# Optimization experiments

Measured on AMD Instinct MI355X. Metric: run time of the kernel, lower is better.

The kernel has to match this reference:

```python
import jax, jax.numpy as jnp
import numpy as np

N = 50000   # nodes
E = 800000  # edges (avg degree 16)
F_IN = 128
D_HID = 128
N_CLASS = 40


def setup_inputs() -> dict:
    key = jax.random.key(0)
    ks = jax.random.split(key, 10)
    s = 0.05
    return {
        "x": jax.random.normal(ks[0], (N, F_IN), jnp.float32),
        "edge_index": jax.random.randint(ks[1], (2, E), 0, N, dtype=jnp.int32),
        "W_in": jax.random.normal(ks[2], (F_IN, D_HID), jnp.float32) * s,
        "b_in": jnp.zeros((D_HID,), jnp.float32),
        "W1": jax.random.normal(ks[3], (D_HID, D_HID), jnp.float32) * s,
        "b1": jnp.zeros((D_HID,), jnp.float32),
        "W2": jax.random.normal(ks[4], (D_HID, D_HID), jnp.float32) * s,
        "b2": jnp.zeros((D_HID,), jnp.float32),
        "W_out": jax.random.normal(ks[5], (D_HID, N_CLASS), jnp.float32) * s,
        "b_out": jnp.zeros((N_CLASS,), jnp.float32),
    }


def _gcn_norm(edge_index, num_nodes):
    # Add self loops, compute symmetric normalization D^-1/2 (A+I) D^-1/2.
    loop = jnp.arange(num_nodes, dtype=edge_index.dtype)
    src = jnp.concatenate([edge_index[0], loop])
    dst = jnp.concatenate([edge_index[1], loop])
    deg = jnp.zeros((num_nodes,), jnp.float32).at[dst].add(1.0)
    dinv = jnp.where(deg > 0, jax.lax.rsqrt(deg), 0.0)
    norm = dinv[src] * dinv[dst]  # [E+N]
    return src, dst, norm


def _gcn_conv(h, W, b, src, dst, norm, num_nodes):
    # transform then sparse aggregate (gather-scale-scatter)
    h = h @ W                                   # [N, d]
    msg = h[src] * norm[:, None]                # [E+N, d]
    agg = jax.ops.segment_sum(msg, dst, num_segments=num_nodes)
    return agg + b


def reference(x, edge_index, W_in, b_in, W1, b1, W2, b2, W_out, b_out):
    num_nodes = x.shape[0]
    src, dst, norm = _gcn_norm(edge_index, num_nodes)
    h = _gcn_conv(x, W_in, b_in, src, dst, norm, num_nodes)
    # eval mode: dropout is identity
    h = jax.nn.relu(_gcn_conv(h, W1, b1, src, dst, norm, num_nodes))
    h = jax.nn.relu(_gcn_conv(h, W2, b2, src, dst, norm, num_nodes))
    out = h @ W_out + b_out
    return jax.nn.log_softmax(out, axis=1)
```

## Files before the change

kernel.cpp:

```cpp
#include <hip/hip_runtime.h>
#include <hip/hip_bf16.h>
#include <math.h>

typedef unsigned int uint;
typedef unsigned short ushort;
typedef __attribute__((ext_vector_type(8))) short short8;
typedef __attribute__((ext_vector_type(4))) float f32x4;

__device__ __forceinline__ float bf_lo(uint u) { return __uint_as_float(u << 16); }
__device__ __forceinline__ float bf_hi(uint u) { return __uint_as_float(u & 0xffff0000u); }
__device__ __forceinline__ ushort f2bf(float f) {
  __hip_bfloat16 h = __float2bfloat16(f);
  return *reinterpret_cast<ushort*>(&h);
}
__device__ __forceinline__ uint pack2(float a, float b) {
  return (uint)f2bf(a) | ((uint)f2bf(b) << 16);
}

__global__ __launch_bounds__(256) void k_pcnt(
    const float* __restrict__ W_in, const float* __restrict__ W1,
    const float* __restrict__ W2, ushort* __restrict__ Wt,
    const int* __restrict__ edges, int* __restrict__ cnt8, int E, int n)
{
  int b = blockIdx.x;
  if (b < 24) {
    const float* W = (b < 8) ? W_in : (b < 16) ? W1 : W2;
    ushort* dst = Wt + (size_t)(b >> 3) * 16384;
    int id = (b & 7) * 256 + threadIdx.x;
    int col = id >> 4, kc = id & 15;
    const float* src = W + (size_t)(kc * 8) * 128 + col;
    uint4 pk;
    pk.x = pack2(src[0],       src[128]);
    pk.y = pack2(src[2 * 128], src[3 * 128]);
    pk.z = pack2(src[4 * 128], src[5 * 128]);
    pk.w = pack2(src[6 * 128], src[7 * 128]);
    ((uint4*)dst)[id] = pk;
  } else {
    int cb = b - 24;
    int* my = cnt8 + (size_t)(cb & 7) * n;
    int stride = ((int)gridDim.x - 24) * 256;
    for (int e = cb * 256 + threadIdx.x; e < E; e += stride)
      atomicAdd(&my[edges[E + e]], 1);
  }
}

__global__ void k_scan1(const int* __restrict__ cnt8, int* __restrict__ cnt,
                        int* __restrict__ incl, int* __restrict__ bsum,
                        float* __restrict__ dinv, int n) {
  __shared__ int s[256];
  int tid = threadIdx.x;
  int gid = blockIdx.x * 256 + tid;
  int x = 0;
  if (gid < n) {
    #pragma unroll
    for (int p = 0; p < 8; ++p) x += cnt8[(size_t)p * n + gid];
    cnt[gid] = x;
    dinv[gid] = rsqrtf((float)x + 1.0f);
  }
  s[tid] = x;
  __syncthreads();
  #pragma unroll
  for (int off = 1; off < 256; off <<= 1) {
    int t = (tid >= off) ? s[tid - off] : 0;
    __syncthreads();
    x += t; s[tid] = x;
    __syncthreads();
  }
  incl[gid] = x;
  if (tid == 255) bsum[blockIdx.x] = x;
}

__global__ void k_scan3(const int* __restrict__ incl, const int* __restrict__ cnt,
                        const int* __restrict__ bsum, int* __restrict__ offs,
                        int* __restrict__ curs, int n, int E, int nb) {
  __shared__ int sb[256];
  int tid = threadIdx.x;
  sb[tid] = (tid < (int)blockIdx.x && tid < nb) ? bsum[tid] : 0;
  __syncthreads();
  #pragma unroll
  for (int off = 128; off; off >>= 1) {
    if (tid < off) sb[tid] += sb[tid + off];
    __syncthreads();
  }
  int base = sb[0];
  int gid = blockIdx.x * 256 + tid;
  if (gid < n) {
    int v = incl[gid] - cnt[gid] + base;
    offs[gid] = v;
    curs[gid] = v;
  }
  if (gid == 0) offs[n] = E;
}

__global__ __launch_bounds__(256) void k_gf(
    const float* __restrict__ A, const ushort* __restrict__ Wt,
    const float* __restrict__ dinv, ushort* __restrict__ T, int n, int gb,
    const int* __restrict__ edges, int* __restrict__ curs,
    int* __restrict__ csr, int E, int npp, int nbp)
{
  __shared__ ushort sW[128 * 128];
  int tid = threadIdx.x;

  if ((int)blockIdx.x >= gb) {
    int b2 = blockIdx.x - gb;
    int part = b2 & 7;
    int lo = part * npp, hi = lo + npp;
    for (int e = (b2 >> 3) * 256 + tid; e < E; e += nbp * 256) {
      int d = edges[E + e];
      if (d >= lo && d < hi) {
        int s = edges[e];
        int pos = atomicAdd(&curs[d], 1);
        csr[pos] = s;
      }
    }
    return;
  }

  {
    const uint4* Wt4 = (const uint4*)Wt;
    uint4* sW4 = (uint4*)sW;
    #pragma unroll
    for (int j = 0; j < 8; ++j) {
      int id = j * 256 + tid;
      int col = id >> 4, kc = id & 15;
      sW4[(col << 4) | (kc ^ (col & 7))] = Wt4[id];
    }
  }
  __syncthreads();

  int wid = tid >> 6, lane = tid & 63;
  int lr = lane & 15, lg = lane >> 4;
  int rbase = blockIdx.x * 64 + wid * 16;
  int arow = rbase + lr;
  bool valid = arow < n;

  f32x4 acc[8];
  #pragma unroll
  for (int cf = 0; cf < 8; ++cf) acc[cf] = (f32x4){0.f, 0.f, 0.f, 0.f};

  #pragma unroll
  for (int ks = 0; ks < 4; ++ks) {
    short8 a = {};
    if (valid) {
      const float4* Af = (const float4*)(A + (size_t)arow * 128) + (ks * 4 + lg) * 2;
      float4 u = Af[0], w = Af[1];
      union { uint4 u4; short8 s8; } cv;
      cv.u4.x = pack2(u.x, u.y); cv.u4.y = pack2(u.z, u.w);
      cv.u4.z = pack2(w.x, w.y); cv.u4.w = pack2(w.z, w.w);
      a = cv.s8;
    }
    int kc = (ks << 2) | lg;
    #pragma unroll
    for (int cf = 0; cf < 8; ++cf) {
      int col = (cf << 4) | lr;
      const short8* bp = (const short8*)sW + ((col << 4) | (kc ^ (lr & 7)));
      acc[cf] = __builtin_amdgcn_mfma_f32_16x16x32_bf16(a, *bp, acc[cf], 0, 0, 0);
    }
  }

  #pragma unroll
  for (int v = 0; v < 4; ++v) {
    int row = rbase + (lg << 2) + v;
    if (row < n) {
      float s = dinv[row];
      ushort* dst = T + (size_t)row * 128 + lr;
      #pragma unroll
      for (int cf = 0; cf < 8; ++cf) dst[cf << 4] = f2bf(acc[cf][v] * s);
    }
  }
}

__global__ __launch_bounds__(256) void k_gemm(
    const ushort* __restrict__ Ap, const ushort* __restrict__ Wt,
    const float* __restrict__ dinv, ushort* __restrict__ T, int n)
{
  __shared__ ushort sW[128 * 128];
  int tid = threadIdx.x;
  {
    const uint4* Wt4 = (const uint4*)Wt;
    uint4* sW4 = (uint4*)sW;
    #pragma unroll
    for (int j = 0; j < 8; ++j) {
      int id = j * 256 + tid;
      int col = id >> 4, kc = id & 15;
      sW4[(col << 4) | (kc ^ (col & 7))] = Wt4[id];
    }
  }
  __syncthreads();

  int wid = tid >> 6, lane = tid & 63;
  int lr = lane & 15, lg = lane >> 4;
  int rbase = blockIdx.x * 64 + wid * 16;
  int arow = rbase + lr;
  bool valid = arow < n;

  f32x4 acc[8];
  #pragma unroll
  for (int cf = 0; cf < 8; ++cf) acc[cf] = (f32x4){0.f, 0.f, 0.f, 0.f};

  #pragma unroll
  for (int ks = 0; ks < 4; ++ks) {
    short8 a = {};
    if (valid) a = ((const short8*)(Ap + (size_t)arow * 128))[ks * 4 + lg];
    int kc = (ks << 2) | lg;
    #pragma unroll
    for (int cf = 0; cf < 8; ++cf) {
      int col = (cf << 4) | lr;
      const short8* bp = (const short8*)sW + ((col << 4) | (kc ^ (lr & 7)));
      acc[cf] = __builtin_amdgcn_mfma_f32_16x16x32_bf16(a, *bp, acc[cf], 0, 0, 0);
    }
  }

  #pragma unroll
  for (int v = 0; v < 4; ++v) {
    int row = rbase + (lg << 2) + v;
    if (row < n) {
      float s = dinv[row];
      ushort* dst = T + (size_t)row * 128 + lr;
      #pragma unroll
      for (int cf = 0; cf < 8; ++cf) dst[cf << 4] = f2bf(acc[cf][v] * s);
    }
  }
}

__global__ __launch_bounds__(256) void k_agg(
    const ushort* __restrict__ T, const int* __restrict__ offs,
    const int* __restrict__ csr, const float* __restrict__ dinv,
    const float* __restrict__ bias, ushort* __restrict__ H, int n, int relu)
{
  int u = (blockIdx.x << 2) + (threadIdx.x >> 6);
  if (u >= n) return;
  int lane = threadIdx.x & 63;
  const uint* Tu = (const uint*)T;
  uint su = Tu[(size_t)u * 64 + lane];
  float ax = bf_lo(su), ay = bf_hi(su);
  int e0 = offs[u], e1 = offs[u + 1];
  int deg = e1 - e0;
  int dcap = deg > 64 ? 64 : deg;
  int eid = (lane < deg) ? csr[e0 + lane] : 0;
  int j = 0;
  for (; j + 8 <= dcap; j += 8) {
    int s0 = __shfl(eid, j);     int s1 = __shfl(eid, j + 1);
    int s2 = __shfl(eid, j + 2); int s3 = __shfl(eid, j + 3);
    int s4 = __shfl(eid, j + 4); int s5 = __shfl(eid, j + 5);
    int s6 = __shfl(eid, j + 6); int s7 = __shfl(eid, j + 7);
    uint v0 = Tu[(size_t)s0 * 64 + lane];
    uint v1 = Tu[(size_t)s1 * 64 + lane];
    uint v2 = Tu[(size_t)s2 * 64 + lane];
    uint v3 = Tu[(size_t)s3 * 64 + lane];
    uint v4 = Tu[(size_t)s4 * 64 + lane];
    uint v5 = Tu[(size_t)s5 * 64 + lane];
    uint v6 = Tu[(size_t)s6 * 64 + lane];
    uint v7 = Tu[(size_t)s7 * 64 + lane];
    ax += ((bf_lo(v0) + bf_lo(v1)) + (bf_lo(v2) + bf_lo(v3))) +
          ((bf_lo(v4) + bf_lo(v5)) + (bf_lo(v6) + bf_lo(v7)));
    ay += ((bf_hi(v0) + bf_hi(v1)) + (bf_hi(v2) + bf_hi(v3))) +
          ((bf_hi(v4) + bf_hi(v5)) + (bf_hi(v6) + bf_hi(v7)));
  }
  for (; j < dcap; ++j) {
    int s = __shfl(eid, j);
    uint v = Tu[(size_t)s * 64 + lane];
    ax += bf_lo(v); ay += bf_hi(v);
  }
  for (int e = e0 + 64; e < e1; ++e) {
    uint v = Tu[(size_t)csr[e] * 64 + lane];
    ax += bf_lo(v); ay += bf_hi(v);
  }
  float du = dinv[u];
  float2 b2 = *(const float2*)(bias + (lane << 1));
  float ox = fmaf(ax, du, b2.x);
  float oy = fmaf(ay, du, b2.y);
  if (relu) { ox = fmaxf(ox, 0.f); oy = fmaxf(oy, 0.f); }
  ((uint*)H)[(size_t)u * 64 + lane] = pack2(ox, oy);
}

__global__ __launch_bounds__(256) void k_head(
    const ushort* __restrict__ H, const float* __restrict__ Wo,
    const float* __restrict__ bo, float* __restrict__ out, int n)
{
  __shared__ float sWo[128 * 40];
  __shared__ float sX[128 * 64];
  int tid = threadIdx.x;
  int rbase = blockIdx.x * 64;

  {
    const float4* Wo4 = (const float4*)Wo;
    float4* sWo4 = (float4*)sWo;
    #pragma unroll
    for (int i = 0; i < 5; ++i) sWo4[i * 256 + tid] = Wo4[i * 256 + tid];
  }
  {
    const uint4* H4 = (const uint4*)H;
    #pragma unroll
    for (int j = 0; j < 4; ++j) {
      int id = j * 256 + tid;
      int r = id & 63, kc8 = id >> 6;
      int row = rbase + r;
      uint4 v = make_uint4(0u, 0u, 0u, 0u);
      if (row < n) v = H4[(size_t)row * 16 + kc8];
      float f[8] = {bf_lo(v.x), bf_hi(v.x), bf_lo(v.y), bf_hi(v.y),
                    bf_lo(v.z), bf_hi(v.z), bf_lo(v.w), bf_hi(v.w)};
      #pragma unroll
      for (int j2 = 0; j2 < 8; ++j2) {
        int k = kc8 * 8 + j2;
        int swz = ((k >> 2) & 7) << 2;
        sX[k * 64 + (r ^ swz)] = f[j2];
      }
    }
  }
  __syncthreads();

  int cg = tid & 7;
  int rg = tid >> 3;
  float bj[5];
  #pragma unroll
  for (int j = 0; j < 5; ++j) bj[j] = bo[cg * 5 + j];
  float acc[2][5];
  #pragma unroll
  for (int i = 0; i < 2; ++i)
    #pragma unroll
    for (int j = 0; j < 5; ++j) acc[i][j] = bj[j];

  #pragma unroll 4
  for (int k = 0; k < 128; ++k) {
    int swz = ((k >> 2) & 7) << 2;
    float2 xv = *(const float2*)(sX + k * 64 + ((rg << 1) ^ swz));
    const float* wr = sWo + k * 40 + cg * 5;
    float w0 = wr[0], w1 = wr[1], w2 = wr[2], w3 = wr[3], w4 = wr[4];
    acc[0][0] = fmaf(xv.x, w0, acc[0][0]);
    acc[0][1] = fmaf(xv.x, w1, acc[0][1]);
    acc[0][2] = fmaf(xv.x, w2, acc[0][2]);
    acc[0][3] = fmaf(xv.x, w3, acc[0][3]);
    acc[0][4] = fmaf(xv.x, w4, acc[0][4]);
    acc[1][0] = fmaf(xv.y, w0, acc[1][0]);
    acc[1][1] = fmaf(xv.y, w1, acc[1][1]);
    acc[1][2] = fmaf(xv.y, w2, acc[1][2]);
    acc[1][3] = fmaf(xv.y, w3, acc[1][3]);
    acc[1][4] = fmaf(xv.y, w4, acc[1][4]);
  }

  #pragma unroll
  for (int i = 0; i < 2; ++i) {
    int row = rbase + (rg << 1) + i;
    float m = acc[i][0];
    m = fmaxf(m, acc[i][1]); m = fmaxf(m, acc[i][2]);
    m = fmaxf(m, acc[i][3]); m = fmaxf(m, acc[i][4]);
    m = fmaxf(m, __shfl_xor(m, 1));
    m = fmaxf(m, __shfl_xor(m, 2));
    m = fmaxf(m, __shfl_xor(m, 4));
    float s = 0.f;
    #pragma unroll
    for (int j = 0; j < 5; ++j) s += __expf(acc[i][j] - m);
    s += __shfl_xor(s, 1);
    s += __shfl_xor(s, 2);
    s += __shfl_xor(s, 4);
    float ls = m + __logf(s);
    if (row < n) {
      float* dst = out + (size_t)row * 40 + cg * 5;
      #pragma unroll
      for (int j = 0; j < 5; ++j) dst[j] = acc[i][j] - ls;
    }
  }
}

extern "C" void kernel_launch(void* const* d_in, const int* in_sizes, int n_in,
                              void* d_out, int out_size, void* d_ws, size_t ws_size,
                              hipStream_t stream) {
  const float* x    = (const float*)d_in[0];
  const int*   edges= (const int*)d_in[1];
  const float* W_in = (const float*)d_in[2];
  const float* b_in = (const float*)d_in[3];
  const float* W1   = (const float*)d_in[4];
  const float* b1   = (const float*)d_in[5];
  const float* W2   = (const float*)d_in[6];
  const float* b2   = (const float*)d_in[7];
  const float* Wo   = (const float*)d_in[8];
  const float* bo   = (const float*)d_in[9];
  float* out = (float*)d_out;

  int N = in_sizes[0] / 128;
  int E = in_sizes[1] / 2;
  int NB = (N + 255) / 256;

  char* p = (char*)d_ws;
  auto alloc = [&](size_t bytes) {
    char* r = p; p += (bytes + 255) & ~(size_t)255; return r;
  };
  ushort* t   = (ushort*)alloc((size_t)N * 128 * 2);
  ushort* h   = (ushort*)alloc((size_t)N * 128 * 2);
  ushort* wt  = (ushort*)alloc(3 * 16384 * 2);
  int*   cnt8 = (int*)  alloc((size_t)N * 8 * 4);
  int*   cnt  = (int*)  alloc((size_t)N * 4);
  float* dinv = (float*)alloc((size_t)N * 4);
  int*   incl = (int*)  alloc((size_t)NB * 256 * 4);
  int*   bsum = (int*)  alloc(256 * 4);
  int*   offs = (int*)  alloc((size_t)(N + 1) * 4);
  int*   curs = (int*)  alloc((size_t)N * 4);
  int*   csr  = (int*)  alloc((size_t)E * 4);
  (void)ws_size; (void)n_in; (void)out_size;

  int NPP = (N + 7) / 8;
  int NBP = 512;
  int GB = (N + 63) / 64;
  int AB = (N + 3) / 4;

  hipMemsetAsync(cnt8, 0, (size_t)N * 8 * 4, stream);
  k_pcnt <<<24 + 2048, 256, 0, stream>>>(W_in, W1, W2, wt, edges, cnt8, E, N);
  k_scan1<<<NB, 256, 0, stream>>>(cnt8, cnt, incl, bsum, dinv, N);
  k_scan3<<<NB, 256, 0, stream>>>(incl, cnt, bsum, offs, curs, N, E, NB);
  k_gf   <<<GB + NBP * 8, 256, 0, stream>>>(x, wt, dinv, t, N, GB,
                                            edges, curs, csr, E, NPP, NBP);
  k_agg  <<<AB, 256, 0, stream>>>(t, offs, csr, dinv, b_in, h, N, 0);
  k_gemm <<<GB, 256, 0, stream>>>(h, wt + 16384, dinv, t, N);
  k_agg  <<<AB, 256, 0, stream>>>(t, offs, csr, dinv, b1, h, N, 1);
  k_gemm <<<GB, 256, 0, stream>>>(h, wt + 2 * 16384, dinv, t, N);
  k_agg  <<<AB, 256, 0, stream>>>(t, offs, csr, dinv, b2, h, N, 1);

  k_head <<<GB, 256, 0, stream>>>(h, Wo, bo, out, N);
}
```

Measured before the change: 235.1 us.

## Fuse output head into last aggregation and partition-interleave block-to-row mapping

Removes the separate head kernel by computing the 128x40 output projection and log-softmax inside the final aggregation kernel, one wavefront per node, which avoids writing and re-reading the last hidden layer. GEMM and aggregation blocks now map to rows via blockIdx&7 partitions padded to 64-row multiples. This likely aims to match the XCD round-robin scheduling so each die's L2 holds a contiguous slice of nodes. The CSR fill loop is unrolled 4x to issue more independent loads. The fused head reloads 20KB of Wo per 4-node block and leaves lanes 40-63 idle, which may cost more than the kernel and traffic it removes.

```diff
diff --git a/kernel.cpp b/kernel.cpp
--- a/kernel.cpp
+++ b/kernel.cpp
@@ -2,6 +2,7 @@
 #include <hip/hip_bf16.h>
 #include <math.h>
 
+#define NEG_INF (-3.402823466e38f)
 typedef unsigned int uint;
 typedef unsigned short ushort;
 typedef __attribute__((ext_vector_type(8))) short short8;
@@ -96,7 +97,7 @@
     const float* __restrict__ A, const ushort* __restrict__ Wt,
     const float* __restrict__ dinv, ushort* __restrict__ T, int n, int gb,
     const int* __restrict__ edges, int* __restrict__ curs,
-    int* __restrict__ csr, int E, int npp, int nbp)
+    int* __restrict__ csr, int E, int npart, int nbp)
 {
   __shared__ ushort sW[128 * 128];
   int tid = threadIdx.x;
@@ -104,14 +105,22 @@
   if ((int)blockIdx.x >= gb) {
     int b2 = blockIdx.x - gb;
     int part = b2 & 7;
-    int lo = part * npp, hi = lo + npp;
-    for (int e = (b2 >> 3) * 256 + tid; e < E; e += nbp * 256) {
+    int lo = part * npart, hi = lo + npart;
+    int stride = nbp * 256;
+    int e = (b2 >> 3) * 256 + tid;
+    for (; e + 3 * stride < E; e += 4 * stride) {
+      int d0 = edges[E + e];
+      int d1 = edges[E + e + stride];
+      int d2 = edges[E + e + 2 * stride];
+      int d3 = edges[E + e + 3 * stride];
+      if (d0 >= lo && d0 < hi) { int s = edges[e];              csr[atomicAdd(&curs[d0], 1)] = s; }
+      if (d1 >= lo && d1 < hi) { int s = edges[e + stride];     csr[atomicAdd(&curs[d1], 1)] = s; }
+      if (d2 >= lo && d2 < hi) { int s = edges[e + 2 * stride]; csr[atomicAdd(&curs[d2], 1)] = s; }
+      if (d3 >= lo && d3 < hi) { int s = edges[e + 3 * stride]; csr[atomicAdd(&curs[d3], 1)] = s; }
+    }
+    for (; e < E; e += stride) {
       int d = edges[E + e];
-      if (d >= lo && d < hi) {
-        int s = edges[e];
-        int pos = atomicAdd(&curs[d], 1);
-        csr[pos] = s;
-      }
+      if (d >= lo && d < hi) { int s = edges[e]; csr[atomicAdd(&curs[d], 1)] = s; }
     }
     return;
   }
@@ -130,7 +139,8 @@
 
   int wid = tid >> 6, lane = tid & 63;
   int lr = lane & 15, lg = lane >> 4;
-  int rbase = blockIdx.x * 64 + wid * 16;
+  int part = blockIdx.x & 7, local = blockIdx.x >> 3;
+  int rbase = part * npart + local * 64 + wid * 16;
   int arow = rbase + lr;
   bool valid = arow < n;
 
@@ -172,7 +182,7 @@
 
 __global__ __launch_bounds__(256) void k_gemm(
     const ushort* __restrict__ Ap, const ushort* __restrict__ Wt,
-    const float* __restrict__ dinv, ushort* __restrict__ T, int n)
+    const float* __restrict__ dinv, ushort* __restrict__ T, int n, int npart)
 {
   __shared__ ushort sW[128 * 128];
   int tid = threadIdx.x;
@@ -190,7 +200,8 @@
 
   int wid = tid >> 6, lane = tid & 63;
   int lr = lane & 15, lg = lane >> 4;
-  int rbase = blockIdx.x * 64 + wid * 16;
+  int part = blockIdx.x & 7, local = blockIdx.x >> 3;
+  int rbase = part * npart + local * 64 + wid * 16;
   int arow = rbase + lr;
   bool valid = arow < n;
 
@@ -223,143 +234,93 @@
   }
 }
 
+template <int RELU, int HEAD>
 __global__ __launch_bounds__(256) void k_agg(
     const ushort* __restrict__ T, const int* __restrict__ offs,
     const int* __restrict__ csr, const float* __restrict__ dinv,
-    const float* __restrict__ bias, ushort* __restrict__ H, int n, int relu)
+    const float* __restrict__ bias, ushort* __restrict__ H,
+    const float* __restrict__ Wo, const float* __restrict__ bo,
+    float* __restrict__ outp, int n, int npart)
 {
-  int u = (blockIdx.x << 2) + (threadIdx.x >> 6);
-  if (u >= n) return;
-  int lane = threadIdx.x & 63;
-  const uint* Tu = (const uint*)T;
-  uint su = Tu[(size_t)u * 64 + lane];
-  float ax = bf_lo(su), ay = bf_hi(su);
-  int e0 = offs[u], e1 = offs[u + 1];
-  int deg = e1 - e0;
-  int dcap = deg > 64 ? 64 : deg;
-  int eid = (lane < deg) ? csr[e0 + lane] : 0;
-  int j = 0;
-  for (; j + 8 <= dcap; j += 8) {
-    int s0 = __shfl(eid, j);     int s1 = __shfl(eid, j + 1);
-    int s2 = __shfl(eid, j + 2); int s3 = __shfl(eid, j + 3);
-    int s4 = __shfl(eid, j + 4); int s5 = __shfl(eid, j + 5);
-    int s6 = __shfl(eid, j + 6); int s7 = __shfl(eid, j + 7);
-    uint v0 = Tu[(size_t)s0 * 64 + lane];
-    uint v1 = Tu[(size_t)s1 * 64 + lane];
-    uint v2 = Tu[(size_t)s2 * 64 + lane];
-    uint v3 = Tu[(size_t)s3 * 64 + lane];
-    uint v4 = Tu[(size_t)s4 * 64 + lane];
-    uint v5 = Tu[(size_t)s5 * 64 + lane];
-    uint v6 = Tu[(size_t)s6 * 64 + lane];
-    uint v7 = Tu[(size_t)s7 * 64 + lane];
-    ax += ((bf_lo(v0) + bf_lo(v1)) + (bf_lo(v2) + bf_lo(v3))) +
-          ((bf_lo(v4) + bf_lo(v5)) + (bf_lo(v6) + bf_lo(v7)));
-    ay += ((bf_hi(v0) + bf_hi(v1)) + (bf_hi(v2) + bf_hi(v3))) +
-          ((bf_hi(v4) + bf_hi(v5)) + (bf_hi(v6) + bf_hi(v7)));
-  }
-  for (; j < dcap; ++j) {
-    int s = __shfl(eid, j);
-    uint v = Tu[(size_t)s * 64 + lane];
-    ax += bf_lo(v); ay += bf_hi(v);
-  }
-  for (int e = e0 + 64; e < e1; ++e) {
-    uint v = Tu[(size_t)csr[e] * 64 + lane];
-    ax += bf_lo(v); ay += bf_hi(v);
-  }
-  float du = dinv[u];
-  float2 b2 = *(const float2*)(bias + (lane << 1));
-  float ox = fmaf(ax, du, b2.x);
-  float oy = fmaf(ay, du, b2.y);
-  if (relu) { ox = fmaxf(ox, 0.f); oy = fmaxf(oy, 0.f); }
-  ((uint*)H)[(size_t)u * 64 + lane] = pack2(ox, oy);
-}
-
-__global__ __launch_bounds__(256) void k_head(
-    const ushort* __restrict__ H, const float* __restrict__ Wo,
-    const float* __restrict__ bo, float* __restrict__ out, int n)
-{
-  __shared__ float sWo[128 * 40];
-  __shared__ float sX[128 * 64];
-  int tid = threadIdx.x;
-  int rbase = blockIdx.x * 64;
-
-  {
-    const float4* Wo4 = (const float4*)Wo;
-    float4* sWo4 = (float4*)sWo;
-    #pragma unroll
-    for (int i = 0; i < 5; ++i) sWo4[i * 256 + tid] = Wo4[i * 256 + tid];
-  }
-  {
-    const uint4* H4 = (const uint4*)H;
-    #pragma unroll
-    for (int j = 0; j < 4; ++j) {
-      int id = j * 256 + tid;
-      int r = id & 63, kc8 = id >> 6;
-      int row = rbase + r;
-      uint4 v = make_uint4(0u, 0u, 0u, 0u);
-      if (row < n) v = H4[(size_t)row * 16 + kc8];
-      float f[8] = {bf_lo(v.x), bf_hi(v.x), bf_lo(v.y), bf_hi(v.y),
-                    bf_lo(v.z), bf_hi(v.z), bf_lo(v.w), bf_hi(v.w)};
+  int tid = threadIdx.x;
+  int lane = tid & 63, wid = tid >> 6;
+  int part = blockIdx.x & 7, local = blockIdx.x >> 3;
+  int u = part * npart + (local << 2) + wid;
+  if (!HEAD && u >= n) return;
+
+  float ox = 0.f, oy = 0.f;
+  if (u < n) {
+    const uint* Tu = (const uint*)T;
+    uint su = Tu[(size_t)u * 64 + lane];
+    float ax = bf_lo(su), ay = bf_hi(su);
+    int e0 = offs[u], e1 = offs[u + 1];
+    int deg = e1 - e0;
+    int dcap = deg > 64 ? 64 : deg;
+    int eid = (lane < deg) ? csr[e0 + lane] : 0;
+    int j = 0;
+    for (; j + 8 <= dcap; j += 8) {
+      int s0 = __shfl(eid, j);     int s1 = __shfl(eid, j + 1);
+      int s2 = __shfl(eid, j + 2); int s3 = __shfl(eid, j + 3);
+      int s4 = __shfl(eid, j + 4); int s5 = __shfl(eid, j + 5);
+      int s6 = __shfl(eid, j + 6); int s7 = __shfl(eid, j + 7);
+      uint v0 = Tu[(size_t)s0 * 64 + lane];
+      uint v1 = Tu[(size_t)s1 * 64 + lane];
+      uint v2 = Tu[(size_t)s2 * 64 + lane];
+      uint v3 = Tu[(size_t)s3 * 64 + lane];
+      uint v4 = Tu[(size_t)s4 * 64 + lane];
+      uint v5 = Tu[(size_t)s5 * 64 + lane];
+      uint v6 = Tu[(size_t)s6 * 64 + lane];
+      uint v7 = Tu[(size_t)s7 * 64 + lane];
+      ax += ((bf_lo(v0) + bf_lo(v1)) + (bf_lo(v2) + bf_lo(v3))) +
+            ((bf_lo(v4) + bf_lo(v5)) + (bf_lo(v6) + bf_lo(v7)));
+      ay += ((bf_hi(v0) + bf_hi(v1)) + (bf_hi(v2) + bf_hi(v3))) +
+            ((bf_hi(v4) + bf_hi(v5)) + (bf_hi(v6) + bf_hi(v7)));
+    }
+    for (; j < dcap; ++j) {
+      int s = __shfl(eid, j);
+      uint v = Tu[(size_t)s * 64 + lane];
+      ax += bf_lo(v); ay += bf_hi(v);
+    }
+    for (int e = e0 + 64; e < e1; ++e) {
+      uint v = Tu[(size_t)csr[e] * 64 + lane];
+      ax += bf_lo(v); ay += bf_hi(v);
+    }
+    float du = dinv[u];
+    float2 b2 = *(const float2*)(bias + (lane << 1));
+    ox = fmaf(ax, du, b2.x);
+    oy = fmaf(ay, du, b2.y);
+    if (RELU) { ox = fmaxf(ox, 0.f); oy = fmaxf(oy, 0.f); }
+  }
+
+  if constexpr (HEAD) {
+    __shared__ float sWo[128 * 40];
+    __shared__ float sH[4][128];
+    for (int i = tid; i < 1280; i += 256) ((float4*)sWo)[i] = ((const float4*)Wo)[i];
+    if (u < n) { sH[wid][lane * 2] = ox; sH[wid][lane * 2 + 1] = oy; }
+    __syncthreads();
+    if (u < n) {
+      int c = (lane < 40) ? lane : 0;
+      float a0 = 0.f, a1 = 0.f, a2 = 0.f, a3 = 0.f;
+      const float* hr = sH[wid];
+      #pragma unroll 8
+      for (int k = 0; k < 128; k += 4) {
+        a0 = fmaf(hr[k],     sWo[k * 40 + c],       a0);
+        a1 = fmaf(hr[k + 1], sWo[(k + 1) * 40 + c], a1);
+        a2 = fmaf(hr[k + 2], sWo[(k + 2) * 40 + c], a2);
+        a3 = fmaf(hr[k + 3], sWo[(k + 3) * 40 + c], a3);
+      }
+      float logit = (a0 + a1) + (a2 + a3) + bo[c];
+      float m = (lane < 40) ? logit : NEG_INF;
       #pragma unroll
-      for (int j2 = 0; j2 < 8; ++j2) {
-        int k = kc8 * 8 + j2;
-        int swz = ((k >> 2) & 7) << 2;
-        sX[k * 64 + (r ^ swz)] = f[j2];
-      }
-    }
-  }
-  __syncthreads();
-
-  int cg = tid & 7;
-  int rg = tid >> 3;
-  float bj[5];
-  #pragma unroll
-  for (int j = 0; j < 5; ++j) bj[j] = bo[cg * 5 + j];
-  float acc[2][5];
-  #pragma unroll
-  for (int i = 0; i < 2; ++i)
-    #pragma unroll
-    for (int j = 0; j < 5; ++j) acc[i][j] = bj[j];
-
-  #pragma unroll 4
-  for (int k = 0; k < 128; ++k) {
-    int swz = ((k >> 2) & 7) << 2;
-    float2 xv = *(const float2*)(sX + k * 64 + ((rg << 1) ^ swz));
-    const float* wr = sWo + k * 40 + cg * 5;
-    float w0 = wr[0], w1 = wr[1], w2 = wr[2], w3 = wr[3], w4 = wr[4];
-    acc[0][0] = fmaf(xv.x, w0, acc[0][0]);
-    acc[0][1] = fmaf(xv.x, w1, acc[0][1]);
-    acc[0][2] = fmaf(xv.x, w2, acc[0][2]);
-    acc[0][3] = fmaf(xv.x, w3, acc[0][3]);
-    acc[0][4] = fmaf(xv.x, w4, acc[0][4]);
-    acc[1][0] = fmaf(xv.y, w0, acc[1][0]);
-    acc[1][1] = fmaf(xv.y, w1, acc[1][1]);
-    acc[1][2] = fmaf(xv.y, w2, acc[1][2]);
-    acc[1][3] = fmaf(xv.y, w3, acc[1][3]);
-    acc[1][4] = fmaf(xv.y, w4, acc[1][4]);
-  }
-
-  #pragma unroll
-  for (int i = 0; i < 2; ++i) {
-    int row = rbase + (rg << 1) + i;
-    float m = acc[i][0];
-    m = fmaxf(m, acc[i][1]); m = fmaxf(m, acc[i][2]);
-    m = fmaxf(m, acc[i][3]); m = fmaxf(m, acc[i][4]);
-    m = fmaxf(m, __shfl_xor(m, 1));
-    m = fmaxf(m, __shfl_xor(m, 2));
-    m = fmaxf(m, __shfl_xor(m, 4));
-    float s = 0.f;
-    #pragma unroll
-    for (int j = 0; j < 5; ++j) s += __expf(acc[i][j] - m);
-    s += __shfl_xor(s, 1);
-    s += __shfl_xor(s, 2);
-    s += __shfl_xor(s, 4);
-    float ls = m + __logf(s);
-    if (row < n) {
-      float* dst = out + (size_t)row * 40 + cg * 5;
+      for (int o = 32; o; o >>= 1) m = fmaxf(m, __shfl_xor(m, o));
+      float ex = (lane < 40) ? __expf(logit - m) : 0.f;
+      float s = ex;
       #pragma unroll
-      for (int j = 0; j < 5; ++j) dst[j] = acc[i][j] - ls;
-    }
+      for (int o = 32; o; o >>= 1) s += __shfl_xor(s, o);
+      if (lane < 40) outp[(size_t)u * 40 + lane] = logit - m - __logf(s);
+    }
+  } else {
+    if (u < n) ((uint*)H)[(size_t)u * 64 + lane] = pack2(ox, oy);
   }
 }
 
@@ -399,22 +360,25 @@
   int*   csr  = (int*)  alloc((size_t)E * 4);
   (void)ws_size; (void)n_in; (void)out_size;
 
-  int NPP = (N + 7) / 8;
+  int NPART = (((N + 7) / 8 + 63) / 64) * 64;
+  int GBP = NPART / 64;
+  int GB  = GBP * 8;
+  int APP = NPART / 4;
+  int AB  = APP * 8;
   int NBP = 512;
-  int GB = (N + 63) / 64;
-  int AB = (N + 3) / 4;
 
   hipMemsetAsync(cnt8, 0, (size_t)N * 8 * 4, stream);
   k_pcnt <<<24 + 2048, 256, 0, stream>>>(W_in, W1, W2, wt, edges, cnt8, E, N);
   k_scan1<<<NB, 256, 0, stream>>>(cnt8, cnt, incl, bsum, dinv, N);
   k_scan3<<<NB, 256, 0, stream>>>(incl, cnt, bsum, offs, curs, N, E, NB);
   k_gf   <<<GB + NBP * 8, 256, 0, stream>>>(x, wt, dinv, t, N, GB,
-                                            edges, curs, csr, E, NPP, NBP);
-  k_agg  <<<AB, 256, 0, stream>>>(t, offs, csr, dinv, b_in, h, N, 0);
-  k_gemm <<<GB, 256, 0, stream>>>(h, wt + 16384, dinv, t, N);
-  k_agg  <<<AB, 256, 0, stream>>>(t, offs, csr, dinv, b1, h, N, 1);
-  k_gemm <<<GB, 256, 0, stream>>>(h, wt + 2 * 16384, dinv, t, N);
-  k_agg  <<<AB, 256, 0, stream>>>(t, offs, csr, dinv, b2, h, N, 1);
-
-  k_head <<<GB, 256, 0, stream>>>(h, Wo, bo, out, N);
-}
+                                            edges, curs, csr, E, NPART, NBP);
+  k_agg<0, 0><<<AB, 256, 0, stream>>>(t, offs, csr, dinv, b_in, h,
+                                      nullptr, nullptr, nullptr, N, NPART);
+  k_gemm <<<GB, 256, 0, stream>>>(h, wt + 16384, dinv, t, N, NPART);
+  k_agg<1, 0><<<AB, 256, 0, stream>>>(t, offs, csr, dinv, b1, h,
+                                      nullptr, nullptr, nullptr, N, NPART);
+  k_gemm <<<GB, 256, 0, stream>>>(h, wt + 2 * 16384, dinv, t, N, NPART);
+  k_agg<1, 1><<<AB, 256, 0, stream>>>(t, offs, csr, dinv, b2, nullptr,
+                                      Wo, bo, out, N, NPART);
+}
```

Result: slower. 256.8 us (+9.2%).

## Reorder fused CSR-fill/GEMM blocks, drop LDS weight staging, template ReLU

Applied to the files above, without the earlier changes.

In the fused k_gf kernel, the CSR scatter blocks now take the low block indices so they are dispatched first, and the GEMM blocks follow. The GEMM path no longer stages the weight matrix into a swizzled LDS tile and reads B fragments straight from global memory, which frees 32KB of shared memory per block and removes a barrier. The scatter loop is unrolled by four so more edge loads are in flight at once. k_agg takes the ReLU flag as a template parameter, which trades extra instantiations for removing a runtime branch. The risks are uncoalesced global loads for the weights, and GEMM blocks possibly waiting behind the long scatter phase.

```diff
diff --git a/kernel.cpp b/kernel.cpp
--- a/kernel.cpp
+++ b/kernel.cpp
@@ -2,6 +2,7 @@
 #include <hip/hip_bf16.h>
 #include <math.h>
 
+#define NEG_INF (-3.402823466e38f)
 typedef unsigned int uint;
 typedef unsigned short ushort;
 typedef __attribute__((ext_vector_type(8))) short short8;
@@ -94,43 +95,38 @@
 
 __global__ __launch_bounds__(256) void k_gf(
     const float* __restrict__ A, const ushort* __restrict__ Wt,
-    const float* __restrict__ dinv, ushort* __restrict__ T, int n, int gb,
+    const float* __restrict__ dinv, ushort* __restrict__ T, int n, int fb,
     const int* __restrict__ edges, int* __restrict__ curs,
     int* __restrict__ csr, int E, int npp, int nbp)
 {
-  __shared__ ushort sW[128 * 128];
   int tid = threadIdx.x;
 
-  if ((int)blockIdx.x >= gb) {
-    int b2 = blockIdx.x - gb;
+  if ((int)blockIdx.x < fb) {
+    int b2 = blockIdx.x;
     int part = b2 & 7;
     int lo = part * npp, hi = lo + npp;
-    for (int e = (b2 >> 3) * 256 + tid; e < E; e += nbp * 256) {
+    int stride = nbp * 256;
+    int e = (b2 >> 3) * 256 + tid;
+    for (; e + 3 * stride < E; e += 4 * stride) {
+      int d0 = edges[E + e];
+      int d1 = edges[E + e + stride];
+      int d2 = edges[E + e + 2 * stride];
+      int d3 = edges[E + e + 3 * stride];
+      if (d0 >= lo && d0 < hi) { int s = edges[e];              csr[atomicAdd(&curs[d0], 1)] = s; }
+      if (d1 >= lo && d1 < hi) { int s = edges[e + stride];     csr[atomicAdd(&curs[d1], 1)] = s; }
+      if (d2 >= lo && d2 < hi) { int s = edges[e + 2 * stride]; csr[atomicAdd(&curs[d2], 1)] = s; }
+      if (d3 >= lo && d3 < hi) { int s = edges[e + 3 * stride]; csr[atomicAdd(&curs[d3], 1)] = s; }
+    }
+    for (; e < E; e += stride) {
       int d = edges[E + e];
-      if (d >= lo && d < hi) {
-        int s = edges[e];
-        int pos = atomicAdd(&curs[d], 1);
-        csr[pos] = s;
-      }
+      if (d >= lo && d < hi) { int s = edges[e]; csr[atomicAdd(&curs[d], 1)] = s; }
     }
     return;
   }
-
-  {
-    const uint4* Wt4 = (const uint4*)Wt;
-    uint4* sW4 = (uint4*)sW;
-    #pragma unroll
-    for (int j = 0; j < 8; ++j) {
-      int id = j * 256 + tid;
-      int col = id >> 4, kc = id & 15;
-      sW4[(col << 4) | (kc ^ (col & 7))] = Wt4[id];
-    }
-  }
-  __syncthreads();
 
   int wid = tid >> 6, lane = tid & 63;
   int lr = lane & 15, lg = lane >> 4;
-  int rbase = blockIdx.x * 64 + wid * 16;
+  int rbase = ((int)blockIdx.x - fb) * 64 + wid * 16;
   int arow = rbase + lr;
   bool valid = arow < n;
 
@@ -153,7 +149,7 @@
     #pragma unroll
     for (int cf = 0; cf < 8; ++cf) {
       int col = (cf << 4) | lr;
-      const short8* bp = (const short8*)sW + ((col << 4) | (kc ^ (lr & 7)));
+      const short8* bp = (const short8*)Wt + ((col << 4) | kc);
       acc[cf] = __builtin_amdgcn_mfma_f32_16x16x32_bf16(a, *bp, acc[cf], 0, 0, 0);
     }
   }
@@ -223,10 +219,11 @@
   }
 }
 
+template <int RELU>
 __global__ __launch_bounds__(256) void k_agg(
     const ushort* __restrict__ T, const int* __restrict__ offs,
     const int* __restrict__ csr, const float* __restrict__ dinv,
-    const float* __restrict__ bias, ushort* __restrict__ H, int n, int relu)
+    const float* __restrict__ bias, ushort* __restrict__ H, int n)
 {
   int u = (blockIdx.x << 2) + (threadIdx.x >> 6);
   if (u >= n) return;
@@ -270,7 +267,7 @@
   float2 b2 = *(const float2*)(bias + (lane << 1));
   float ox = fmaf(ax, du, b2.x);
   float oy = fmaf(ay, du, b2.y);
-  if (relu) { ox = fmaxf(ox, 0.f); oy = fmaxf(oy, 0.f); }
+  if (RELU) { ox = fmaxf(ox, 0.f); oy = fmaxf(oy, 0.f); }
   ((uint*)H)[(size_t)u * 64 + lane] = pack2(ox, oy);
 }
 
@@ -401,20 +398,20 @@
 
   int NPP = (N + 7) / 8;
   int NBP = 512;
-  int GB = (N + 63) / 64;
-  int AB = (N + 3) / 4;
+  int FB  = NBP * 8;
+  int GB  = (N + 63) / 64;
+  int AB  = (N + 3) / 4;
 
   hipMemsetAsync(cnt8, 0, (size_t)N * 8 * 4, stream);
   k_pcnt <<<24 + 2048, 256, 0, stream>>>(W_in, W1, W2, wt, edges, cnt8, E, N);
   k_scan1<<<NB, 256, 0, stream>>>(cnt8, cnt, incl, bsum, dinv, N);
   k_scan3<<<NB, 256, 0, stream>>>(incl, cnt, bsum, offs, curs, N, E, NB);
-  k_gf   <<<GB + NBP * 8, 256, 0, stream>>>(x, wt, dinv, t, N, GB,
-                                            edges, curs, csr, E, NPP, NBP);
-  k_agg  <<<AB, 256, 0, stream>>>(t, offs, csr, dinv, b_in, h, N, 0);
+  k_gf   <<<FB + GB, 256, 0, stream>>>(x, wt, dinv, t, N, FB,
+                                       edges, curs, csr, E, NPP, NBP);
+  k_agg<0><<<AB, 256, 0, stream>>>(t, offs, csr, dinv, b_in, h, N);
   k_gemm <<<GB, 256, 0, stream>>>(h, wt + 16384, dinv, t, N);
-  k_agg  <<<AB, 256, 0, stream>>>(t, offs, csr, dinv, b1, h, N, 1);
+  k_agg<1><<<AB, 256, 0, stream>>>(t, offs, csr, dinv, b1, h, N);
   k_gemm <<<GB, 256, 0, stream>>>(h, wt + 2 * 16384, dinv, t, N);
-  k_agg  <<<AB, 256, 0, stream>>>(t, offs, csr, dinv, b2, h, N, 1);
-
+  k_agg<1><<<AB, 256, 0, stream>>>(t, offs, csr, dinv, b2, h, N);
   k_head <<<GB, 256, 0, stream>>>(h, Wo, bo, out, N);
 }
```

Measured after the change: 251.2 us. 6.9% more time.
